# Optimization experiments

Hardware: AMD Instinct MI355X
Metric: run time of the kernel (lower is better)

## Reference

```python
import jax, jax.numpy as jnp
import numpy as np

B, S, V, L, H, NH, NL = 4, 256, 64, 10, 128, 8, 3
DH = H // NH
LP1 = L + 1


def setup_inputs() -> dict:
    key = jax.random.key(0)
    ks = jax.random.split(key, 18)
    sc = 1.0 / np.sqrt(H)
    return {
        "x": jax.random.normal(ks[0], (B, S, V), jnp.float32),
        "adjacency_logits": jax.random.normal(ks[1], (V, V, LP1), jnp.float32) * 0.1,
        "var_emb": jax.random.normal(ks[2], (V, H), jnp.float32),
        "temp_emb": jax.random.normal(ks[3], (LP1, H), jnp.float32),
        "mech_W": jax.random.normal(ks[4], (V, NL, H, H), jnp.float32) * sc,
        "mech_b": jax.random.normal(ks[5], (V, NL, H), jnp.float32) * 0.01,
        "ln_g": jnp.ones((V, NL, H), jnp.float32),
        "ln_b": jnp.zeros((V, NL, H), jnp.float32),
        "Wq": jax.random.normal(ks[6], (V, H, H), jnp.float32) * sc,
        "Wk": jax.random.normal(ks[7], (V, H, H), jnp.float32) * sc,
        "Wv": jax.random.normal(ks[8], (V, H, H), jnp.float32) * sc,
        "Wo": jax.random.normal(ks[9], (V, H, H), jnp.float32) * sc,
        "bq": jnp.zeros((V, H), jnp.float32),
        "bk": jnp.zeros((V, H), jnp.float32),
        "bv": jnp.zeros((V, H), jnp.float32),
        "bo": jnp.zeros((V, H), jnp.float32),
        "out_W": jax.random.normal(ks[10], (V, H), jnp.float32) * sc,
        "out_b": jnp.zeros((V,), jnp.float32),
    }


def reference(x, adjacency_logits, var_emb, temp_emb, mech_W, mech_b, ln_g, ln_b,
              Wq, Wk, Wv, Wo, bq, bk, bv, bo, out_W, out_b):
    b, s, v = x.shape
    lp1 = adjacency_logits.shape[-1]
    adj = jax.nn.sigmoid(adjacency_logits)  # (V_src, V_tgt, L+1), soft adjacency

    # xlag[b,t,src,l] = x[b, t-l, src] with zero padding (the shift-pad loop, fused)
    xlag = jnp.stack([jnp.pad(x, ((0, 0), (l, 0), (0, 0)))[:, :s] for l in range(lp1)], axis=-1)

    # causal_input[b,t,tgt,h] = sum_{src,l} xlag * adj[src,tgt,l] * (var_emb[src,h] + temp_emb[l,h])
    A = jnp.einsum('btsl,sil->btis', xlag, adj)   # contracted over lag
    Bl = jnp.einsum('btsl,sil->btil', xlag, adj)  # contracted over source
    z = jnp.einsum('btis,sh->btih', A, var_emb) + jnp.einsum('btil,lh->btih', Bl, temp_emb)  # (B,S,V,H)

    # per-variable causal mechanism: Linear -> LayerNorm -> GELU (dropout = identity at eval)
    eps = 1e-5
    nl = mech_W.shape[1]
    for li in range(nl):
        z = jnp.einsum('btvh,vhk->btvk', z, mech_W[:, li]) + mech_b[:, li]
        mu = z.mean(axis=-1, keepdims=True)
        var = z.var(axis=-1, keepdims=True)
        z = (z - mu) / jnp.sqrt(var + eps) * ln_g[:, li] + ln_b[:, li]
        z = jax.nn.gelu(z, approximate=False)

    # per-variable multi-head self-attention over the sequence axis
    def heads(t):
        return t.reshape(b, s, v, NH, DH)
    q = heads(jnp.einsum('btvh,vhk->btvk', z, Wq) + bq)
    k = heads(jnp.einsum('btvh,vhk->btvk', z, Wk) + bk)
    vv = heads(jnp.einsum('btvh,vhk->btvk', z, Wv) + bv)
    scores = jnp.einsum('bqvnd,bkvnd->bvnqk', q, k) / np.sqrt(DH)  # (B,V,NH,S,S)
    attn = jax.nn.softmax(scores, axis=-1)
    o = jnp.einsum('bvnqk,bkvnd->bqvnd', attn, vv).reshape(b, s, v, NH * DH)
    o = jnp.einsum('btvh,vhk->btvk', o, Wo) + bo

    # per-variable output head Linear(H, 1), concatenated over variables
    predictions = jnp.einsum('btvh,vh->btv', o, out_W) + out_b  # (B,S,V)
    return predictions
```

## Files before the change

kernel.cpp:

```cpp
#include <hip/hip_runtime.h>
#include <math.h>

#define BB   4
#define SS   256
#define VV   64
#define LP1  11
#define HH   128
#define NHH  8
#define DHH  16
#define NLL  3
#define BSZ  1024

typedef unsigned short u16;
typedef unsigned int   u32;
typedef __attribute__((ext_vector_type(8))) short s16x8;
typedef __attribute__((ext_vector_type(4))) float f32x4;

__device__ __forceinline__ float bfbits2f(u32 hi16) {
    u32 i = hi16 << 16; float f; __builtin_memcpy(&f, &i, 4); return f;
}
__device__ __forceinline__ u16 f2bf(float f) {
    u32 i; __builtin_memcpy(&i, &f, 4);
    return (u16)((i + 0x7fffu + ((i >> 16) & 1u)) >> 16);
}
__device__ __forceinline__ u16 f2bf_trunc(float f) {
    u32 i; __builtin_memcpy(&i, &f, 4);
    return (u16)(i >> 16);
}
__device__ __forceinline__ float ldf(const void* p, size_t i, int isbf) {
    if (isbf) return bfbits2f(((const u16*)p)[i]);
    return ((const float*)p)[i];
}
__device__ __forceinline__ float4 ld4(const void* p, size_t i, int isbf) {
    float4 v;
    if (isbf) {
        uint2 u = *(const uint2*)((const u16*)p + i);
        v.x = bfbits2f(u.x & 0xffffu); v.y = bfbits2f(u.x >> 16);
        v.z = bfbits2f(u.y & 0xffffu); v.w = bfbits2f(u.y >> 16);
    } else {
        v = *(const float4*)((const float*)p + i);
    }
    return v;
}

__global__ __launch_bounds__(64) void k_sniff(const u16* __restrict__ probe,
                                              int* __restrict__ flags) {
    if (threadIdx.x == 0) {
        int wild = 0;
        for (int j = 0; j < 256; j++) {
            float v = bfbits2f(probe[j]);
            if (!(fabsf(v) < 1e8f)) wild = 1;
        }
        flags[0] = wild ? 0 : 1;
    }
}

__global__ __launch_bounds__(256) void k_adj(const void* __restrict__ logits,
                                             float* __restrict__ adj,
                                             const int* __restrict__ flags) {
    int isbf = flags[0];
    int i = blockIdx.x * 256 + threadIdx.x;
    if (i < VV * VV * LP1) {
        float v = ldf(logits, i, isbf);
        adj[i] = 1.f / (1.f + expf(-v));
    }
}

__global__ __launch_bounds__(128) void k_fuse(const void* __restrict__ Wo,
                                              const void* __restrict__ outW,
                                              const void* __restrict__ bo,
                                              const void* __restrict__ outb,
                                              float* __restrict__ wfused,
                                              float* __restrict__ bfused,
                                              const int* __restrict__ flags) {
    int isbf = flags[0];
    int v = blockIdx.x; int h = threadIdx.x;
    __shared__ float ow[HH];
    __shared__ float red[HH];
    ow[h] = ldf(outW, (size_t)v * HH + h, isbf);
    __syncthreads();
    size_t wb = ((size_t)v * HH + h) * HH;
    float acc = 0.f;
    #pragma unroll 8
    for (int k = 0; k < HH; k++) acc += ldf(Wo, wb + k, isbf) * ow[k];
    wfused[v * HH + h] = acc;
    red[h] = ldf(bo, (size_t)v * HH + h, isbf) * ow[h];
    __syncthreads();
    for (int s = 64; s > 0; s >>= 1) { if (h < s) red[h] += red[h + s]; __syncthreads(); }
    if (h == 0) bfused[v] = red[0] + ldf(outb, v, isbf);
}

__global__ __launch_bounds__(256) void k_causal(const void* __restrict__ x,
                                                const float* __restrict__ adj,
                                                const void* __restrict__ var_emb,
                                                const void* __restrict__ temp_emb,
                                                u16* __restrict__ zh,
                                                u16* __restrict__ zl,
                                                const int* __restrict__ flags) {
    __shared__ float xl[LP1][VV];
    __shared__ float A_sh[VV][VV + 1];
    __shared__ float Blp_sh[VV * LP1 * 4];
    __shared__ float Bl_sh[VV][12];
    int isbf = flags[0];
    int tid = threadIdx.x;
    int bt = blockIdx.x; int b = bt >> 8; int t = bt & 255;

    for (int p = tid; p < LP1 * VV; p += 256) {
        int l = p >> 6, s = p & 63; int tt = t - l;
        xl[l][s] = (tt >= 0) ? ldf(x, (size_t)(b * SS + tt) * VV + s, isbf) : 0.f;
    }
    __syncthreads();

    {
        int i = tid & 63, sg = tid >> 6;
        float blp[LP1];
        #pragma unroll
        for (int l = 0; l < LP1; l++) blp[l] = 0.f;
        for (int k = 0; k < 16; k++) {
            int s = sg + k * 4;
            const float* ap = adj + (s * VV + i) * LP1;
            float a = 0.f;
            #pragma unroll
            for (int l = 0; l < LP1; l++) {
                float pr = xl[l][s] * ap[l];
                a += pr; blp[l] += pr;
            }
            A_sh[i][s] = a;
        }
        #pragma unroll
        for (int l = 0; l < LP1; l++)
            Blp_sh[(i * LP1 + l) * 4 + sg] = blp[l];
    }
    __syncthreads();
    for (int p = tid; p < VV * LP1; p += 256) {
        int i = p / LP1, l = p - i * LP1;
        const float* q = &Blp_sh[(i * LP1 + l) * 4];
        Bl_sh[i][l] = (q[0] + q[1]) + (q[2] + q[3]);
    }
    __syncthreads();

    int h0 = (tid & 31) * 4;
    int ig = tid >> 5;
    float acc[8][4];
    #pragma unroll
    for (int ii = 0; ii < 8; ii++)
        #pragma unroll
        for (int j = 0; j < 4; j++) acc[ii][j] = 0.f;

    if (isbf) {
        for (int s = 0; s < VV; s++) {
            float4 v4 = ld4(var_emb, (size_t)s * HH + h0, 1);
            #pragma unroll
            for (int ii = 0; ii < 8; ii++) {
                float a = A_sh[ig * 8 + ii][s];
                acc[ii][0] += a * v4.x; acc[ii][1] += a * v4.y;
                acc[ii][2] += a * v4.z; acc[ii][3] += a * v4.w;
            }
        }
        #pragma unroll
        for (int l = 0; l < LP1; l++) {
            float4 t4 = ld4(temp_emb, (size_t)l * HH + h0, 1);
            #pragma unroll
            for (int ii = 0; ii < 8; ii++) {
                float bl = Bl_sh[ig * 8 + ii][l];
                acc[ii][0] += bl * t4.x; acc[ii][1] += bl * t4.y;
                acc[ii][2] += bl * t4.z; acc[ii][3] += bl * t4.w;
            }
        }
    } else {
        for (int s = 0; s < VV; s++) {
            float4 v4 = ld4(var_emb, (size_t)s * HH + h0, 0);
            #pragma unroll
            for (int ii = 0; ii < 8; ii++) {
                float a = A_sh[ig * 8 + ii][s];
                acc[ii][0] += a * v4.x; acc[ii][1] += a * v4.y;
                acc[ii][2] += a * v4.z; acc[ii][3] += a * v4.w;
            }
        }
        #pragma unroll
        for (int l = 0; l < LP1; l++) {
            float4 t4 = ld4(temp_emb, (size_t)l * HH + h0, 0);
            #pragma unroll
            for (int ii = 0; ii < 8; ii++) {
                float bl = Bl_sh[ig * 8 + ii][l];
                acc[ii][0] += bl * t4.x; acc[ii][1] += bl * t4.y;
                acc[ii][2] += bl * t4.z; acc[ii][3] += bl * t4.w;
            }
        }
    }

    #pragma unroll
    for (int ii = 0; ii < 8; ii++) {
        int i = ig * 8 + ii;
        size_t idx = ((size_t)i * BSZ + bt) * HH + h0;
        u16 h0_ = f2bf(acc[ii][0]), h1_ = f2bf(acc[ii][1]);
        u16 h2_ = f2bf(acc[ii][2]), h3_ = f2bf(acc[ii][3]);
        uint2 hw, lw;
        hw.x = (u32)h0_ | ((u32)h1_ << 16); hw.y = (u32)h2_ | ((u32)h3_ << 16);
        lw.x = (u32)f2bf(acc[ii][0] - bfbits2f(h0_)) | ((u32)f2bf(acc[ii][1] - bfbits2f(h1_)) << 16);
        lw.y = (u32)f2bf(acc[ii][2] - bfbits2f(h2_)) | ((u32)f2bf(acc[ii][3] - bfbits2f(h3_)) << 16);
        *(uint2*)&zh[idx] = hw;
        *(uint2*)&zl[idx] = lw;
    }
}

struct WPack {
    const void* src[4];
    u16* dh[4];
    u16* dl[4];
};
#define TP 136
__global__ __launch_bounds__(256) void k_wprep(WPack wp,
                                               const int* __restrict__ flags) {
    int isbf = flags[0];
    int mat = blockIdx.x;
    int seg = (mat < 192) ? 0 : 1 + ((mat - 192) >> 6);
    int rel = (mat < 192) ? mat : ((mat - 192) & 63);
    const void* raw = wp.src[seg];
    u16* Wh = wp.dh[seg];
    u16* Wl = wp.dl[seg];
    int tid = threadIdx.x;
    size_t src = (size_t)rel * (HH * HH);
    if (isbf) {
        __shared__ u16 tile[HH * TP];
        const uint4* sp = (const uint4*)((const u16*)raw + src);
        #pragma unroll
        for (int u = 0; u < 8; u++) {
            int p = u * 256 + tid;
            int h = p >> 4, k8 = (p & 15) * 8;
            int k8s = k8 ^ ((((u32)h >> 3) & 15) * 8);
            *(uint4*)&tile[h * TP + k8s] = sp[p];
        }
        __syncthreads();
        #pragma unroll
        for (int u = 0; u < 8; u++) {
            int p = u * 256 + tid;
            int kcol = p >> 4, h8 = (p & 15) * 8;
            u16 vals[8];
            #pragma unroll
            for (int j = 0; j < 8; j++) {
                int h = h8 + j;
                int ks = kcol ^ ((((u32)h >> 3) & 15) * 8);
                vals[j] = tile[h * TP + ks];
            }
            uint4 pk;
            pk.x = (u32)vals[0] | ((u32)vals[1] << 16);
            pk.y = (u32)vals[2] | ((u32)vals[3] << 16);
            pk.z = (u32)vals[4] | ((u32)vals[5] << 16);
            pk.w = (u32)vals[6] | ((u32)vals[7] << 16);
            *(uint4*)&Wh[src + (size_t)kcol * HH + h8] = pk;
        }
    } else {
        int kcol = tid >> 1, h0 = (tid & 1) * 64;
        size_t dst = src + (size_t)kcol * HH;
        for (int i = 0; i < 64; i++) {
            int h = h0 + i;
            float w = ldf(raw, src + (size_t)h * HH + kcol, 0);
            u16 hi = f2bf(w);
            Wh[dst + h] = hi;
            Wl[dst + h] = f2bf(w - bfbits2f(hi));
        }
    }
}

#define LDW 40
__global__ __launch_bounds__(256) void k_gemm(
    const u16* __restrict__ zh, const u16* __restrict__ zl,
    const u16* __restrict__ Wh, const u16* __restrict__ Wl,
    int nper, int li,
    const void* __restrict__ bias, int bias_base, int bias_stride,
    const void* __restrict__ lngp, const void* __restrict__ lnbp,
    int ln_base, int ln_stride,
    void* __restrict__ out1, void* __restrict__ out2, int mode,
    const int* __restrict__ flags)
{
    __shared__ u16 Ah_s[64 * LDW];
    __shared__ u16 Al_s[64 * LDW];
    __shared__ u16 Bh_s[128 * LDW];
    __shared__ u16 Bl_s[128 * LDW];
    int isbf = flags[0];
    int wexact = isbf;
    int tid = threadIdx.x;
    int tile = blockIdx.x, v = blockIdx.y;
    int wave = tid >> 6, lane = tid & 63;
    int quad = lane >> 4, l15 = lane & 15;

    size_t zbase = ((size_t)v * BSZ + (size_t)tile * 64) * HH;
    size_t wbase = (size_t)(v * nper + li) * (HH * HH);

    f32x4 acc[8];
    #pragma unroll
    for (int nt = 0; nt < 8; nt++) {
        f32x4 z = {0.f, 0.f, 0.f, 0.f};
        acc[nt] = z;
    }

    for (int c = 0; c < 4; c++) {
        __syncthreads();
        {
            int row = tid >> 2, k16 = tid & 3;
            size_t src = zbase + (size_t)row * HH + c * 32 + k16 * 8;
            *(uint4*)&Ah_s[row * LDW + k16 * 8] = *(const uint4*)&zh[src];
            *(uint4*)&Al_s[row * LDW + k16 * 8] = *(const uint4*)&zl[src];
        }
        #pragma unroll
        for (int u = 0; u < 2; u++) {
            int p = u * 256 + tid;
            int n = p >> 2, k8 = p & 3;
            *(uint4*)&Bh_s[n * LDW + k8 * 8] =
                *(const uint4*)&Wh[wbase + (size_t)n * HH + c * 32 + k8 * 8];
        }
        if (!wexact) {
            #pragma unroll
            for (int u = 0; u < 2; u++) {
                int p = u * 256 + tid;
                int n = p >> 2, k8 = p & 3;
                *(uint4*)&Bl_s[n * LDW + k8 * 8] =
                    *(const uint4*)&Wl[wbase + (size_t)n * HH + c * 32 + k8 * 8];
            }
        }
        __syncthreads();

        int m0 = wave * 16;
        s16x8 ah = *(const s16x8*)&Ah_s[(m0 + l15) * LDW + quad * 8];
        s16x8 al = *(const s16x8*)&Al_s[(m0 + l15) * LDW + quad * 8];
        if (wexact) {
            #pragma unroll
            for (int nt = 0; nt < 8; nt++) {
                s16x8 bh = *(const s16x8*)&Bh_s[(nt * 16 + l15) * LDW + quad * 8];
                acc[nt] = __builtin_amdgcn_mfma_f32_16x16x32_bf16(ah, bh, acc[nt], 0, 0, 0);
                acc[nt] = __builtin_amdgcn_mfma_f32_16x16x32_bf16(al, bh, acc[nt], 0, 0, 0);
            }
        } else {
            #pragma unroll
            for (int nt = 0; nt < 8; nt++) {
                s16x8 bh = *(const s16x8*)&Bh_s[(nt * 16 + l15) * LDW + quad * 8];
                s16x8 bl = *(const s16x8*)&Bl_s[(nt * 16 + l15) * LDW + quad * 8];
                acc[nt] = __builtin_amdgcn_mfma_f32_16x16x32_bf16(ah, bh, acc[nt], 0, 0, 0);
                acc[nt] = __builtin_amdgcn_mfma_f32_16x16x32_bf16(al, bh, acc[nt], 0, 0, 0);
                acc[nt] = __builtin_amdgcn_mfma_f32_16x16x32_bf16(ah, bl, acc[nt], 0, 0, 0);
            }
        }
    }

    float bcol[8], gcol[8], b2col[8];
    #pragma unroll
    for (int nt = 0; nt < 8; nt++) {
        int col = nt * 16 + l15;
        bcol[nt] = ldf(bias, (size_t)bias_base + (size_t)v * bias_stride + col, isbf);
        if (mode == 2) {
            gcol[nt]  = ldf(lngp, (size_t)ln_base + (size_t)v * ln_stride + col, isbf);
            b2col[nt] = ldf(lnbp, (size_t)ln_base + (size_t)v * ln_stride + col, isbf);
        }
    }
    #pragma unroll
    for (int r = 0; r < 4; r++) {
        float vals[8];
        float sum = 0.f, sq = 0.f;
        #pragma unroll
        for (int nt = 0; nt < 8; nt++) {
            float val = acc[nt][r] + bcol[nt];
            vals[nt] = val; sum += val; sq += val * val;
        }
        if (mode == 2) {
            #pragma unroll
            for (int m = 1; m < 16; m <<= 1) {
                sum += __shfl_xor(sum, m);
                sq  += __shfl_xor(sq, m);
            }
            float mean = sum * (1.f / HH);
            float var  = sq * (1.f / HH) - mean * mean;
            float rstd = rsqrtf(var + 1e-5f);
            #pragma unroll
            for (int nt = 0; nt < 8; nt++) {
                float y = (vals[nt] - mean) * rstd * gcol[nt] + b2col[nt];
                vals[nt] = 0.5f * y * (1.f + erff(y * 0.70710678118654752f));
            }
        }
        int row = tile * 64 + wave * 16 + quad * 4 + r;
        size_t ob = ((size_t)v * BSZ + row) * HH;
        if (mode == 1) {
            u16* o16 = (u16*)out1;
            #pragma unroll
            for (int nt = 0; nt < 8; nt++) o16[ob + nt * 16 + l15] = f2bf(vals[nt]);
        } else if (mode == 3) {
            u16* o16 = (u16*)out1;
            int bb = row >> 8, tt = row & 255;
            #pragma unroll
            for (int nt = 0; nt < 8; nt++)
                o16[(((size_t)(v * BB + bb) * NHH + nt) * DHH + l15) * SS + tt] = f2bf(vals[nt]);
        } else {
            u16* oh = (u16*)out1; u16* ol = (u16*)out2;
            #pragma unroll
            for (int nt = 0; nt < 8; nt++) {
                u16 hi = f2bf(vals[nt]);
                oh[ob + nt * 16 + l15] = hi;
                ol[ob + nt * 16 + l15] = f2bf(vals[nt] - bfbits2f(hi));
            }
        }
    }
}

__global__ __launch_bounds__(256) void k_attn2(const u16* __restrict__ Qh,
                                               const u16* __restrict__ Ql,
                                               const u16* __restrict__ K16,
                                               const u16* __restrict__ Vt,
                                               float* __restrict__ O) {
    __shared__ u16 Kp_sh[SS * LDW];
    __shared__ u16 Vt_sh[DHH * 264];
    __shared__ u16 P_sh[4][16 * LDW];
    int tid = threadIdx.x;
    int wave = tid >> 6, lane = tid & 63;
    int quad = lane >> 4, l15 = lane & 15;
    int bn = blockIdx.x, v = blockIdx.y;
    int b = bn >> 3, n = bn & 7;
    size_t qkbase = ((size_t)v * BSZ + b * SS) * HH + n * DHH;
    size_t vtbase = ((size_t)(v * BB + b) * NHH + n) * DHH * SS;

    {
        int row = tid;
        uint4 k0 = *(const uint4*)&K16[qkbase + (size_t)row * HH];
        uint4 k1 = *(const uint4*)&K16[qkbase + (size_t)row * HH + 8];
        *(uint4*)&Kp_sh[row * LDW + 0]  = k0;
        *(uint4*)&Kp_sh[row * LDW + 8]  = k1;
        *(uint4*)&Kp_sh[row * LDW + 16] = k0;
        *(uint4*)&Kp_sh[row * LDW + 24] = k1;
    }
    #pragma unroll
    for (int u = 0; u < 2; u++) {
        int p = u * 256 + tid;
        int d = p >> 5, su = (p & 31) * 8;
        *(uint4*)&Vt_sh[d * 264 + su] = *(const uint4*)&Vt[vtbase + (size_t)d * SS + su];
    }
    __syncthreads();

    s16x8 ones;
    #pragma unroll
    for (int i = 0; i < 8; i++) ones[i] = (short)0x3F80;

    for (int mt = wave * 4; mt < wave * 4 + 4; mt++) {
        const u16* Qsrc = (quad < 2) ? Qh : Ql;
        s16x8 aq = *(const s16x8*)&Qsrc[qkbase + (size_t)(mt * 16 + l15) * HH + (quad & 1) * 8];
        f32x4 oacc = {0.f, 0.f, 0.f, 0.f};
        f32x4 lacc = {0.f, 0.f, 0.f, 0.f};
        for (int jt2 = 0; jt2 < 8; jt2++) {
            #pragma unroll
            for (int sub = 0; sub < 2; sub++) {
                int jt = jt2 * 2 + sub;
                s16x8 bk = *(const s16x8*)&Kp_sh[(jt * 16 + l15) * LDW + quad * 8];
                f32x4 s = {0.f, 0.f, 0.f, 0.f};
                s = __builtin_amdgcn_mfma_f32_16x16x32_bf16(aq, bk, s, 0, 0, 0);
                #pragma unroll
                for (int r = 0; r < 4; r++) {
                    float p = __expf(s[r] * 0.25f);
                    P_sh[wave][(quad * 4 + r) * LDW + sub * 16 + l15] = f2bf_trunc(p);
                }
            }
            s16x8 ap = *(const s16x8*)&P_sh[wave][l15 * LDW + quad * 8];
            s16x8 bv = *(const s16x8*)&Vt_sh[l15 * 264 + jt2 * 32 + quad * 8];
            oacc = __builtin_amdgcn_mfma_f32_16x16x32_bf16(ap, bv, oacc, 0, 0, 0);
            lacc = __builtin_amdgcn_mfma_f32_16x16x32_bf16(ap, ones, lacc, 0, 0, 0);
        }
        #pragma unroll
        for (int r = 0; r < 4; r++) {
            float val = oacc[r] / lacc[r];
            O[((size_t)v * BSZ + b * SS + mt * 16 + quad * 4 + r) * HH + n * DHH + l15] = val;
        }
    }
}

__global__ __launch_bounds__(256) void k_final(const float* __restrict__ o,
                                               const float* __restrict__ wfused,
                                               const float* __restrict__ bfused,
                                               void* __restrict__ out,
                                               const int* __restrict__ flags) {
    __shared__ float wf[HH];
    int isbf = flags[0];
    int tid = threadIdx.x; int b = blockIdx.x; int v = blockIdx.y;
    if (tid < HH) wf[tid] = wfused[v * HH + tid];
    __syncthreads();
    int rg = tid >> 3;
    int l8 = tid & 7;
    float4 w0 = *(const float4*)&wf[l8 * 16];
    float4 w1 = *(const float4*)&wf[l8 * 16 + 4];
    float4 w2 = *(const float4*)&wf[l8 * 16 + 8];
    float4 w3 = *(const float4*)&wf[l8 * 16 + 12];
    float bv = bfused[v];
    #pragma unroll
    for (int pass = 0; pass < 8; pass++) {
        int bt = b * SS + pass * 32 + rg;
        const float4* orow = (const float4*)(o + ((size_t)v * BSZ + bt) * HH + l8 * 16);
        float4 a0 = orow[0], a1 = orow[1], a2 = orow[2], a3 = orow[3];
        float acc = a0.x * w0.x + a0.y * w0.y + a0.z * w0.z + a0.w * w0.w
                  + a1.x * w1.x + a1.y * w1.y + a1.z * w1.z + a1.w * w1.w
                  + a2.x * w2.x + a2.y * w2.y + a2.z * w2.z + a2.w * w2.w
                  + a3.x * w3.x + a3.y * w3.y + a3.z * w3.z + a3.w * w3.w;
        acc += __shfl_xor(acc, 1);
        acc += __shfl_xor(acc, 2);
        acc += __shfl_xor(acc, 4);
        if (l8 == 0) {
            float pred = acc + bv;
            size_t oi = (size_t)bt * VV + v;
            if (isbf) ((u16*)out)[oi] = f2bf(pred);
            else      ((float*)out)[oi] = pred;
        }
    }
}

extern "C" void kernel_launch(void* const* d_in, const int* in_sizes, int n_in,
                              void* d_out, int out_size, void* d_ws, size_t ws_size,
                              hipStream_t stream) {
    (void)out_size; (void)ws_size;

    static const int dict_sizes[18]  = {65536,45056,8192,1408,3145728,24576,24576,24576,
                                        1048576,1048576,1048576,1048576,8192,8192,8192,8192,8192,64};
    static const int alpha_sizes[18] = {1048576,1048576,1048576,1048576,45056,8192,8192,8192,
                                        8192,24576,24576,3145728,24576,8192,64,1408,8192,65536};
    static const int alpha_pos[18]   = {17,4,16,15,11,12,10,9,2,0,3,1,7,5,8,6,13,14};
    static const int alpha_logical[18] = {9,11,8,10,1,13,15,12,14,7,6,4,5,16,17,3,2,0};

    const void* in[18];
    bool is_dict = (n_in == 18), is_alpha = (n_in == 18);
    for (int i = 0; i < 18 && i < n_in; i++) {
        if (in_sizes[i] != dict_sizes[i])  is_dict = false;
        if (in_sizes[i] != alpha_sizes[i]) is_alpha = false;
    }
    if (is_dict) {
        for (int i = 0; i < 18; i++) in[i] = d_in[i];
    } else if (is_alpha) {
        for (int i = 0; i < 18; i++) in[i] = d_in[alpha_pos[i]];
    } else {
        bool used[18] = {false};
        for (int a = 0; a < 18; a++) {
            int lg = alpha_logical[a];
            for (int i = 0; i < n_in && i < 18; i++) {
                if (!used[i] && in_sizes[i] == dict_sizes[lg]) {
                    in[lg] = d_in[i]; used[i] = true; break;
                }
            }
        }
    }

    const void* x        = in[0];
    const void* adjl     = in[1];
    const void* var_emb  = in[2];
    const void* temp_emb = in[3];
    const void* mechW    = in[4];
    const void* mechb    = in[5];
    const void* lng      = in[6];
    const void* lnb      = in[7];
    const void* Wq       = in[8];
    const void* Wk       = in[9];
    const void* Wv       = in[10];
    const void* Wo       = in[11];
    const void* bq       = in[12];
    const void* bk       = in[13];
    const void* bv       = in[14];
    const void* bo       = in[15];
    const void* outW     = in[16];
    const void* outb     = in[17];

    float* ws     = (float*)d_ws;
    int*   flags  = (int*)ws;
    float* adj    = ws + 32;
    float* wfused = ws + 45088;
    float* bfused = ws + 53280;
    u16*   zhA    = (u16*)(ws + 53376);
    u16*   zlA    = (u16*)(ws + 4247680);
    u16*   zhB    = (u16*)(ws + 8441984);
    u16*   zlB    = (u16*)(ws + 12636288);
    float* Obuf   = ws + 8441984;
    u16*   K16    = (u16*)(ws + 16830592);
    u16*   Vt16   = (u16*)(ws + 21024896);
    u16*   WtmH   = (u16*)(ws + 25219200);
    u16*   WtmL   = (u16*)(ws + 26792064);
    u16*   WtqH   = (u16*)(ws + 28364928);
    u16*   WtqL   = (u16*)(ws + 28889216);
    u16*   WtkH   = (u16*)(ws + 29413504);
    u16*   WtkL   = (u16*)(ws + 29937792);
    u16*   WtvH   = (u16*)(ws + 30462080);
    u16*   WtvL   = (u16*)(ws + 30986368);

    k_sniff <<<dim3(1),    dim3(64),  0, stream>>>((const u16*)mechW, flags);
    k_adj   <<<dim3(176),  dim3(256), 0, stream>>>(adjl, adj, flags);
    k_fuse  <<<dim3(64),   dim3(128), 0, stream>>>(Wo, outW, bo, outb, wfused, bfused, flags);
    k_causal<<<dim3(BSZ),  dim3(256), 0, stream>>>(x, adj, var_emb, temp_emb, zhA, zlA, flags);

    WPack wp;
    wp.src[0] = mechW; wp.dh[0] = WtmH; wp.dl[0] = WtmL;
    wp.src[1] = Wq;    wp.dh[1] = WtqH; wp.dl[1] = WtqL;
    wp.src[2] = Wk;    wp.dh[2] = WtkH; wp.dl[2] = WtkL;
    wp.src[3] = Wv;    wp.dh[3] = WtvH; wp.dl[3] = WtvL;
    k_wprep <<<dim3(384),  dim3(256), 0, stream>>>(wp, flags);

    k_gemm<<<dim3(16, 64), dim3(256), 0, stream>>>(zhA, zlA, WtmH, WtmL, NLL, 0,
            mechb, 0 * HH, NLL * HH, lng, lnb, 0 * HH, NLL * HH, zhB, zlB, 2, flags);
    k_gemm<<<dim3(16, 64), dim3(256), 0, stream>>>(zhB, zlB, WtmH, WtmL, NLL, 1,
            mechb, 1 * HH, NLL * HH, lng, lnb, 1 * HH, NLL * HH, zhA, zlA, 2, flags);
    k_gemm<<<dim3(16, 64), dim3(256), 0, stream>>>(zhA, zlA, WtmH, WtmL, NLL, 2,
            mechb, 2 * HH, NLL * HH, lng, lnb, 2 * HH, NLL * HH, zhB, zlB, 2, flags);

    k_gemm<<<dim3(16, 64), dim3(256), 0, stream>>>(zhB, zlB, WtqH, WtqL, 1, 0,
            bq, 0, HH, lng, lnb, 0, 0, zhA, zlA, 4, flags);
    k_gemm<<<dim3(16, 64), dim3(256), 0, stream>>>(zhB, zlB, WtkH, WtkL, 1, 0,
            bk, 0, HH, lng, lnb, 0, 0, K16, (void*)0, 1, flags);
    k_gemm<<<dim3(16, 64), dim3(256), 0, stream>>>(zhB, zlB, WtvH, WtvL, 1, 0,
            bv, 0, HH, lng, lnb, 0, 0, Vt16, (void*)0, 3, flags);

    k_attn2 <<<dim3(BB * NHH, VV), dim3(256), 0, stream>>>(zhA, zlA, K16, Vt16, Obuf);
    k_final <<<dim3(BB, VV), dim3(256), 0, stream>>>(Obuf, wfused, bfused, d_out, flags);
}
```

Before: 445.9 us.

## Fuse mechanism MLP layers and QKV projections into one LDS-resident megakernel

Replaces six separate GEMM launches (three mechanism layers plus Q, K, V projections) with one kernel. Each block keeps its 64-row hi/lo activation tile in shared memory across all layers and writes only the final Q, K and V-transposed outputs to global memory. This removes the per-layer global write and read of intermediate activations, and five launches. Weights are now staged in 64-wide K chunks instead of 32-wide. The cost is a much larger shared-memory footprint, which lowers occupancy, and a serial per-block chain of six GEMMs.

Result: faster. 399.7 us (-10.3%).

```diff
diff --git a/kernel.cpp b/kernel.cpp
--- a/kernel.cpp
+++ b/kernel.cpp
@@ -263,144 +263,170 @@
     }
 }
 
-#define LDW 40
-__global__ __launch_bounds__(256) void k_gemm(
+#define PZ 136
+#define PB 72
+__global__ __launch_bounds__(256) void k_mega(
     const u16* __restrict__ zh, const u16* __restrict__ zl,
-    const u16* __restrict__ Wh, const u16* __restrict__ Wl,
-    int nper, int li,
-    const void* __restrict__ bias, int bias_base, int bias_stride,
-    const void* __restrict__ lngp, const void* __restrict__ lnbp,
-    int ln_base, int ln_stride,
-    void* __restrict__ out1, void* __restrict__ out2, int mode,
+    const u16* __restrict__ WmH, const u16* __restrict__ WmL,
+    const u16* __restrict__ WqH, const u16* __restrict__ WqL,
+    const u16* __restrict__ WkH, const u16* __restrict__ WkL,
+    const u16* __restrict__ WvH, const u16* __restrict__ WvL,
+    const void* __restrict__ mechb,
+    const void* __restrict__ lng, const void* __restrict__ lnb,
+    const void* __restrict__ bq, const void* __restrict__ bk,
+    const void* __restrict__ bv,
+    u16* __restrict__ Qh, u16* __restrict__ Ql,
+    u16* __restrict__ Ko, u16* __restrict__ Vt,
     const int* __restrict__ flags)
 {
-    __shared__ u16 Ah_s[64 * LDW];
-    __shared__ u16 Al_s[64 * LDW];
-    __shared__ u16 Bh_s[128 * LDW];
-    __shared__ u16 Bl_s[128 * LDW];
+    __shared__ u16 Az_h[64 * PZ];
+    __shared__ u16 Az_l[64 * PZ];
+    __shared__ u16 Bh_s[128 * PB];
+    __shared__ u16 Bl_s[128 * PB];
     int isbf = flags[0];
     int wexact = isbf;
     int tid = threadIdx.x;
     int tile = blockIdx.x, v = blockIdx.y;
     int wave = tid >> 6, lane = tid & 63;
     int quad = lane >> 4, l15 = lane & 15;
+    int m0 = wave * 16;
 
     size_t zbase = ((size_t)v * BSZ + (size_t)tile * 64) * HH;
-    size_t wbase = (size_t)(v * nper + li) * (HH * HH);
-
-    f32x4 acc[8];
     #pragma unroll
-    for (int nt = 0; nt < 8; nt++) {
-        f32x4 z = {0.f, 0.f, 0.f, 0.f};
-        acc[nt] = z;
-    }
-
-    for (int c = 0; c < 4; c++) {
-        __syncthreads();
-        {
-            int row = tid >> 2, k16 = tid & 3;
-            size_t src = zbase + (size_t)row * HH + c * 32 + k16 * 8;
-            *(uint4*)&Ah_s[row * LDW + k16 * 8] = *(const uint4*)&zh[src];
-            *(uint4*)&Al_s[row * LDW + k16 * 8] = *(const uint4*)&zl[src];
-        }
-        #pragma unroll
-        for (int u = 0; u < 2; u++) {
-            int p = u * 256 + tid;
-            int n = p >> 2, k8 = p & 3;
-            *(uint4*)&Bh_s[n * LDW + k8 * 8] =
-                *(const uint4*)&Wh[wbase + (size_t)n * HH + c * 32 + k8 * 8];
-        }
-        if (!wexact) {
-            #pragma unroll
-            for (int u = 0; u < 2; u++) {
+    for (int u = 0; u < 4; u++) {
+        int idx = u * 256 + tid;
+        int row = idx >> 4, k8 = (idx & 15) * 8;
+        *(uint4*)&Az_h[row * PZ + k8] = *(const uint4*)&zh[zbase + (size_t)row * HH + k8];
+        *(uint4*)&Az_l[row * PZ + k8] = *(const uint4*)&zl[zbase + (size_t)row * HH + k8];
+    }
+
+    for (int li = 0; li < 6; li++) {
+        const u16* Wh; const u16* Wl; size_t wbase;
+        if (li < 3)       { Wh = WmH; Wl = WmL; wbase = (size_t)(v * NLL + li) * (HH * HH); }
+        else if (li == 3) { Wh = WqH; Wl = WqL; wbase = (size_t)v * (HH * HH); }
+        else if (li == 4) { Wh = WkH; Wl = WkL; wbase = (size_t)v * (HH * HH); }
+        else              { Wh = WvH; Wl = WvL; wbase = (size_t)v * (HH * HH); }
+
+        f32x4 acc[8];
+        #pragma unroll
+        for (int nt = 0; nt < 8; nt++) {
+            f32x4 zz = {0.f, 0.f, 0.f, 0.f};
+            acc[nt] = zz;
+        }
+
+        for (int c = 0; c < 2; c++) {
+            __syncthreads();
+            #pragma unroll
+            for (int u = 0; u < 4; u++) {
                 int p = u * 256 + tid;
-                int n = p >> 2, k8 = p & 3;
-                *(uint4*)&Bl_s[n * LDW + k8 * 8] =
-                    *(const uint4*)&Wl[wbase + (size_t)n * HH + c * 32 + k8 * 8];
-            }
-        }
-        __syncthreads();
-
-        int m0 = wave * 16;
-        s16x8 ah = *(const s16x8*)&Ah_s[(m0 + l15) * LDW + quad * 8];
-        s16x8 al = *(const s16x8*)&Al_s[(m0 + l15) * LDW + quad * 8];
-        if (wexact) {
+                int n = p >> 3, k8 = (p & 7) * 8;
+                *(uint4*)&Bh_s[n * PB + k8] =
+                    *(const uint4*)&Wh[wbase + (size_t)n * HH + c * 64 + k8];
+            }
+            if (!wexact) {
+                #pragma unroll
+                for (int u = 0; u < 4; u++) {
+                    int p = u * 256 + tid;
+                    int n = p >> 3, k8 = (p & 7) * 8;
+                    *(uint4*)&Bl_s[n * PB + k8] =
+                        *(const uint4*)&Wl[wbase + (size_t)n * HH + c * 64 + k8];
+                }
+            }
+            __syncthreads();
+
+            #pragma unroll
+            for (int kk = 0; kk < 2; kk++) {
+                int ka = c * 64 + kk * 32 + quad * 8;
+                int kb = kk * 32 + quad * 8;
+                s16x8 ah = *(const s16x8*)&Az_h[(m0 + l15) * PZ + ka];
+                s16x8 al = *(const s16x8*)&Az_l[(m0 + l15) * PZ + ka];
+                if (wexact) {
+                    #pragma unroll
+                    for (int nt = 0; nt < 8; nt++) {
+                        s16x8 bh = *(const s16x8*)&Bh_s[(nt * 16 + l15) * PB + kb];
+                        acc[nt] = __builtin_amdgcn_mfma_f32_16x16x32_bf16(ah, bh, acc[nt], 0, 0, 0);
+                        acc[nt] = __builtin_amdgcn_mfma_f32_16x16x32_bf16(al, bh, acc[nt], 0, 0, 0);
+                    }
+                } else {
+                    #pragma unroll
+                    for (int nt = 0; nt < 8; nt++) {
+                        s16x8 bh = *(const s16x8*)&Bh_s[(nt * 16 + l15) * PB + kb];
+                        s16x8 bl = *(const s16x8*)&Bl_s[(nt * 16 + l15) * PB + kb];
+                        acc[nt] = __builtin_amdgcn_mfma_f32_16x16x32_bf16(ah, bh, acc[nt], 0, 0, 0);
+                        acc[nt] = __builtin_amdgcn_mfma_f32_16x16x32_bf16(al, bh, acc[nt], 0, 0, 0);
+                        acc[nt] = __builtin_amdgcn_mfma_f32_16x16x32_bf16(ah, bl, acc[nt], 0, 0, 0);
+                    }
+                }
+            }
+        }
+
+        float bcol[8], gcol[8], b2col[8];
+        #pragma unroll
+        for (int nt = 0; nt < 8; nt++) {
+            int col = nt * 16 + l15;
+            if (li < 3) {
+                size_t pb = (size_t)v * (NLL * HH) + (size_t)li * HH + col;
+                bcol[nt]  = ldf(mechb, pb, isbf);
+                gcol[nt]  = ldf(lng, pb, isbf);
+                b2col[nt] = ldf(lnb, pb, isbf);
+            } else {
+                const void* bp = (li == 3) ? bq : (li == 4) ? bk : bv;
+                bcol[nt] = ldf(bp, (size_t)v * HH + col, isbf);
+            }
+        }
+        #pragma unroll
+        for (int r = 0; r < 4; r++) {
+            float vals[8];
+            float sum = 0.f, sq = 0.f;
             #pragma unroll
             for (int nt = 0; nt < 8; nt++) {
-                s16x8 bh = *(const s16x8*)&Bh_s[(nt * 16 + l15) * LDW + quad * 8];
-                acc[nt] = __builtin_amdgcn_mfma_f32_16x16x32_bf16(ah, bh, acc[nt], 0, 0, 0);
-                acc[nt] = __builtin_amdgcn_mfma_f32_16x16x32_bf16(al, bh, acc[nt], 0, 0, 0);
-            }
-        } else {
-            #pragma unroll
-            for (int nt = 0; nt < 8; nt++) {
-                s16x8 bh = *(const s16x8*)&Bh_s[(nt * 16 + l15) * LDW + quad * 8];
-                s16x8 bl = *(const s16x8*)&Bl_s[(nt * 16 + l15) * LDW + quad * 8];
-                acc[nt] = __builtin_amdgcn_mfma_f32_16x16x32_bf16(ah, bh, acc[nt], 0, 0, 0);
-                acc[nt] = __builtin_amdgcn_mfma_f32_16x16x32_bf16(al, bh, acc[nt], 0, 0, 0);
-                acc[nt] = __builtin_amdgcn_mfma_f32_16x16x32_bf16(ah, bl, acc[nt], 0, 0, 0);
-            }
-        }
-    }
-
-    float bcol[8], gcol[8], b2col[8];
-    #pragma unroll
-    for (int nt = 0; nt < 8; nt++) {
-        int col = nt * 16 + l15;
-        bcol[nt] = ldf(bias, (size_t)bias_base + (size_t)v * bias_stride + col, isbf);
-        if (mode == 2) {
-            gcol[nt]  = ldf(lngp, (size_t)ln_base + (size_t)v * ln_stride + col, isbf);
-            b2col[nt] = ldf(lnbp, (size_t)ln_base + (size_t)v * ln_stride + col, isbf);
-        }
-    }
-    #pragma unroll
-    for (int r = 0; r < 4; r++) {
-        float vals[8];
-        float sum = 0.f, sq = 0.f;
-        #pragma unroll
-        for (int nt = 0; nt < 8; nt++) {
-            float val = acc[nt][r] + bcol[nt];
-            vals[nt] = val; sum += val; sq += val * val;
-        }
-        if (mode == 2) {
-            #pragma unroll
-            for (int m = 1; m < 16; m <<= 1) {
-                sum += __shfl_xor(sum, m);
-                sq  += __shfl_xor(sq, m);
-            }
-            float mean = sum * (1.f / HH);
-            float var  = sq * (1.f / HH) - mean * mean;
-            float rstd = rsqrtf(var + 1e-5f);
-            #pragma unroll
-            for (int nt = 0; nt < 8; nt++) {
-                float y = (vals[nt] - mean) * rstd * gcol[nt] + b2col[nt];
-                vals[nt] = 0.5f * y * (1.f + erff(y * 0.70710678118654752f));
-            }
-        }
-        int row = tile * 64 + wave * 16 + quad * 4 + r;
-        size_t ob = ((size_t)v * BSZ + row) * HH;
-        if (mode == 1) {
-            u16* o16 = (u16*)out1;
-            #pragma unroll
-            for (int nt = 0; nt < 8; nt++) o16[ob + nt * 16 + l15] = f2bf(vals[nt]);
-        } else if (mode == 3) {
-            u16* o16 = (u16*)out1;
-            int bb = row >> 8, tt = row & 255;
-            #pragma unroll
-            for (int nt = 0; nt < 8; nt++)
-                o16[(((size_t)(v * BB + bb) * NHH + nt) * DHH + l15) * SS + tt] = f2bf(vals[nt]);
-        } else {
-            u16* oh = (u16*)out1; u16* ol = (u16*)out2;
-            #pragma unroll
-            for (int nt = 0; nt < 8; nt++) {
-                u16 hi = f2bf(vals[nt]);
-                oh[ob + nt * 16 + l15] = hi;
-                ol[ob + nt * 16 + l15] = f2bf(vals[nt] - bfbits2f(hi));
-            }
-        }
-    }
-}
-
+                float val = acc[nt][r] + bcol[nt];
+                vals[nt] = val; sum += val; sq += val * val;
+            }
+            int rloc = m0 + quad * 4 + r;
+            if (li < 3) {
+                #pragma unroll
+                for (int m = 1; m < 16; m <<= 1) {
+                    sum += __shfl_xor(sum, m);
+                    sq  += __shfl_xor(sq, m);
+                }
+                float mean = sum * (1.f / HH);
+                float var  = sq * (1.f / HH) - mean * mean;
+                float rstd = rsqrtf(var + 1e-5f);
+                #pragma unroll
+                for (int nt = 0; nt < 8; nt++) {
+                    float y = (vals[nt] - mean) * rstd * gcol[nt] + b2col[nt];
+                    y = 0.5f * y * (1.f + erff(y * 0.70710678118654752f));
+                    u16 hi = f2bf(y);
+                    Az_h[rloc * PZ + nt * 16 + l15] = hi;
+                    Az_l[rloc * PZ + nt * 16 + l15] = f2bf(y - bfbits2f(hi));
+                }
+            } else {
+                int row = tile * 64 + rloc;
+                size_t ob = ((size_t)v * BSZ + row) * HH;
+                if (li == 3) {
+                    #pragma unroll
+                    for (int nt = 0; nt < 8; nt++) {
+                        u16 hi = f2bf(vals[nt]);
+                        Qh[ob + nt * 16 + l15] = hi;
+                        Ql[ob + nt * 16 + l15] = f2bf(vals[nt] - bfbits2f(hi));
+                    }
+                } else if (li == 4) {
+                    #pragma unroll
+                    for (int nt = 0; nt < 8; nt++)
+                        Ko[ob + nt * 16 + l15] = f2bf(vals[nt]);
+                } else {
+                    int bb = row >> 8, tt = row & 255;
+                    #pragma unroll
+                    for (int nt = 0; nt < 8; nt++)
+                        Vt[(((size_t)(v * BB + bb) * NHH + nt) * DHH + l15) * SS + tt] = f2bf(vals[nt]);
+                }
+            }
+        }
+    }
+}
+
+#define LDW 40
 __global__ __launch_bounds__(256) void k_attn2(const u16* __restrict__ Qh,
                                                const u16* __restrict__ Ql,
                                                const u16* __restrict__ K16,
@@ -569,7 +595,7 @@
     u16*   zlA    = (u16*)(ws + 4247680);
     u16*   zhB    = (u16*)(ws + 8441984);
     u16*   zlB    = (u16*)(ws + 12636288);
-    float* Obuf   = ws + 8441984;
+    float* Obuf   = ws + 53376;
     u16*   K16    = (u16*)(ws + 16830592);
     u16*   Vt16   = (u16*)(ws + 21024896);
     u16*   WtmH   = (u16*)(ws + 25219200);
@@ -593,20 +619,12 @@
     wp.src[3] = Wv;    wp.dh[3] = WtvH; wp.dl[3] = WtvL;
     k_wprep <<<dim3(384),  dim3(256), 0, stream>>>(wp, flags);
 
-    k_gemm<<<dim3(16, 64), dim3(256), 0, stream>>>(zhA, zlA, WtmH, WtmL, NLL, 0,
-            mechb, 0 * HH, NLL * HH, lng, lnb, 0 * HH, NLL * HH, zhB, zlB, 2, flags);
-    k_gemm<<<dim3(16, 64), dim3(256), 0, stream>>>(zhB, zlB, WtmH, WtmL, NLL, 1,
-            mechb, 1 * HH, NLL * HH, lng, lnb, 1 * HH, NLL * HH, zhA, zlA, 2, flags);
-    k_gemm<<<dim3(16, 64), dim3(256), 0, stream>>>(zhA, zlA, WtmH, WtmL, NLL, 2,
-            mechb, 2 * HH, NLL * HH, lng, lnb, 2 * HH, NLL * HH, zhB, zlB, 2, flags);
-
-    k_gemm<<<dim3(16, 64), dim3(256), 0, stream>>>(zhB, zlB, WtqH, WtqL, 1, 0,
-            bq, 0, HH, lng, lnb, 0, 0, zhA, zlA, 4, flags);
-    k_gemm<<<dim3(16, 64), dim3(256), 0, stream>>>(zhB, zlB, WtkH, WtkL, 1, 0,
-            bk, 0, HH, lng, lnb, 0, 0, K16, (void*)0, 1, flags);
-    k_gemm<<<dim3(16, 64), dim3(256), 0, stream>>>(zhB, zlB, WtvH, WtvL, 1, 0,
-            bv, 0, HH, lng, lnb, 0, 0, Vt16, (void*)0, 3, flags);
-
-    k_attn2 <<<dim3(BB * NHH, VV), dim3(256), 0, stream>>>(zhA, zlA, K16, Vt16, Obuf);
+    k_mega<<<dim3(16, 64), dim3(256), 0, stream>>>(
+            zhA, zlA,
+            WtmH, WtmL, WtqH, WtqL, WtkH, WtkL, WtvH, WtvL,
+            mechb, lng, lnb, bq, bk, bv,
+            zhB, zlB, K16, Vt16, flags);
+
+    k_attn2 <<<dim3(BB * NHH, VV), dim3(256), 0, stream>>>(zhB, zlB, K16, Vt16, Obuf);
     k_final <<<dim3(BB, VV), dim3(256), 0, stream>>>(Obuf, wfused, bfused, d_out, flags);
 }
```
